# Kernel tuning notes

Measured on AMD Instinct MI355X. Metric: run time of the kernel, lower is better.

## Reference

```python
import jax, jax.numpy as jnp
import numpy as np

B, C, COUT, HEADS = 1, 256, 256, 8
H, W, KS = 96, 96, 7  # spatial dims and neighborhood kernel size


def _nbr_1d(n, k):
    # NATTEN/flex-mask style clamped window: center = clip(q, wl, n-1-wr)
    wl = k // 2
    wr = k // 2 + (k % 2 - 1)
    q = np.arange(n)
    center = np.clip(q, wl, n - 1 - wr)
    start = center - wl  # in [0, n-k]; window always fully in-bounds
    return start[:, None] + np.arange(k)[None, :]  # [n, k]


def _nbr_idx(h, w, k):
    ih = _nbr_1d(h, k)  # [h, k]
    iw = _nbr_1d(w, k)  # [w, k]
    flat = ih[:, None, :, None] * w + iw[None, :, None, :]  # [h, w, k, k]
    return jnp.asarray(flat.reshape(h * w, k * k))  # [S, K]


def setup_inputs() -> dict:
    key = jax.random.key(0)
    ks = jax.random.split(key, 4)
    x = jax.random.normal(ks[0], (B, C, H, W), jnp.float32)
    w_qkv = jax.random.normal(ks[1], (3 * C, C), jnp.float32) * (C ** -0.5)
    b_qkv = jnp.zeros((3 * C,), jnp.float32)
    w_out = jax.random.normal(ks[2], (COUT, C), jnp.float32) * (C ** -0.5)
    b_out = jnp.zeros((COUT,), jnp.float32)
    return {"x": x, "w_qkv": w_qkv, "b_qkv": b_qkv, "w_out": w_out, "b_out": b_out}


def reference(x, w_qkv, b_qkv, w_out, b_out):
    dh = C // HEADS
    S = H * W
    xl = jnp.moveaxis(x, 1, -1)  # [B,H,W,C]
    qkv = xl @ w_qkv.T + b_qkv  # [B,H,W,3C], layout (qkv, heads, dh) on last axis
    qkv = qkv.reshape(B, S, 3, HEADS, dh)
    q = jnp.transpose(qkv[:, :, 0], (0, 2, 1, 3))  # [B,heads,S,dh]
    k = jnp.transpose(qkv[:, :, 1], (0, 2, 1, 3))
    v = jnp.transpose(qkv[:, :, 2], (0, 2, 1, 3))
    # rope_embed_fraction = 0.0 -> RoPE is identity
    nbr = _nbr_idx(H, W, KS)  # [S, K] static neighbor indices, K = KS*KS
    k_nb = jnp.take(k, nbr, axis=2)  # [B,heads,S,K,dh]
    v_nb = jnp.take(v, nbr, axis=2)  # [B,heads,S,K,dh]
    scores = jnp.einsum('bhsd,bhskd->bhsk', q, k_nb) * (dh ** -0.5)
    attn = jax.nn.softmax(scores, axis=-1)  # window fully in-bounds -> no mask
    out = jnp.einsum('bhsk,bhskd->bhsd', attn, v_nb)  # [B,heads,S,dh]
    out = jnp.transpose(out, (0, 2, 1, 3)).reshape(B, S, HEADS * dh)
    out = out @ w_out.T + b_out  # [B,S,COUT]
    out = out.reshape(B, H, W, COUT)
    return jnp.moveaxis(out, -1, 1)  # [B,COUT,H,W]
```

## Files before the change

### kernel.cpp

```cpp
#include <hip/hip_runtime.h>
#include <hip/hip_bf16.h>
#include <math.h>

#define SD 9216
#define HH 96
#define CC 256
#define NO 768
#define NH 8
#define DH 32
#define NW1 (NO * CC)
#define NWT (NW1 + CC * CC)
#define PROW 232

typedef short bf16x8 __attribute__((ext_vector_type(8)));
typedef short short8v __attribute__((ext_vector_type(8)));
typedef float f32x4 __attribute__((ext_vector_type(4)));
typedef unsigned short us8 __attribute__((ext_vector_type(8)));

__device__ __forceinline__ float bf2f(unsigned short u) {
  union { unsigned u; float f; } c; c.u = ((unsigned)u) << 16; return c.f;
}
__device__ __forceinline__ unsigned short f2bf(float f) {
  unsigned u = __float_as_uint(f);
  unsigned r = (u + 0x7FFF + ((u >> 16) & 1)) >> 16;
  return (unsigned short)r;
}

__global__ __launch_bounds__(256) void prep(const float* __restrict__ x,
                                            const float* __restrict__ wq,
                                            const float* __restrict__ wo,
                                            unsigned short* __restrict__ xbt,
                                            unsigned short* __restrict__ wdst) {
  __shared__ float tile[32][33];
  const int b = blockIdx.x;
  const int t = threadIdx.x;
  if (b < 2304) {
    const int s0 = (b % 288) * 32;
    const int c0 = (b / 288) * 32;
    {
      const int c = t >> 3, s4 = (t & 7) * 4;
      const float4 v = *(const float4*)(x + (size_t)(c0 + c) * SD + s0 + s4);
      tile[c][s4] = v.x; tile[c][s4 + 1] = v.y; tile[c][s4 + 2] = v.z; tile[c][s4 + 3] = v.w;
    }
    __syncthreads();
    {
      const int s = t >> 3, c4 = (t & 7) * 4;
      ushort4 o;
      o.x = f2bf(tile[c4][s]);     o.y = f2bf(tile[c4 + 1][s]);
      o.z = f2bf(tile[c4 + 2][s]); o.w = f2bf(tile[c4 + 3][s]);
      *(ushort4*)(xbt + (size_t)(s0 + s) * CC + c0 + c4) = o;
    }
  } else {
    const int i = ((b - 2304) * 256 + t) * 4;
    if (i < NWT) {
      const float* src = (i < NW1) ? (wq + i) : (wo + (i - NW1));
      const float4 v = *(const float4*)src;
      ushort4 o;
      o.x = f2bf(v.x); o.y = f2bf(v.y); o.z = f2bf(v.z); o.w = f2bf(v.w);
      *(ushort4*)(wdst + i) = o;
    }
  }
}

template <int EPI>
__global__ __launch_bounds__(256) void gemm_mfma(const unsigned short* __restrict__ A,
                                                 const unsigned short* __restrict__ Bm,
                                                 const float* __restrict__ bias,
                                                 void* __restrict__ out) {
  __shared__ short Asd[128 * 40];
  __shared__ short Bsd[128 * 40];
  const int t = threadIdx.x;
  const int m0 = blockIdx.x * 128;
  const int n0 = blockIdx.y * 128;
  const int lane = t & 63;
  const int w = t >> 6;
  const int wm = (w >> 1) * 64, wn = (w & 1) * 64;
  f32x4 acc[4][4] = {};
  const int r0 = t >> 2, c16 = (t & 3) * 8;

  for (int k0 = 0; k0 < CC; k0 += 32) {
#pragma unroll
    for (int i = 0; i < 2; ++i) {
      const int r = i * 64 + r0;
      *(int4*)&Asd[r * 40 + c16] = *(const int4*)(A + (size_t)(m0 + r) * CC + k0 + c16);
      *(int4*)&Bsd[r * 40 + c16] = *(const int4*)(Bm + (size_t)(n0 + r) * CC + k0 + c16);
    }
    __syncthreads();
    const int lr = lane & 15, lk = (lane >> 4) * 8;
    bf16x8 af[4], bf[4];
#pragma unroll
    for (int i = 0; i < 4; ++i) af[i] = *(const bf16x8*)&Asd[(wm + i * 16 + lr) * 40 + lk];
#pragma unroll
    for (int j = 0; j < 4; ++j) bf[j] = *(const bf16x8*)&Bsd[(wn + j * 16 + lr) * 40 + lk];
#pragma unroll
    for (int i = 0; i < 4; ++i)
#pragma unroll
      for (int j = 0; j < 4; ++j)
        acc[i][j] = __builtin_amdgcn_mfma_f32_16x16x32_bf16(af[i], bf[j], acc[i][j], 0, 0, 0);
    __syncthreads();
  }

  const int lc = lane & 15, lr4 = (lane >> 4) * 4;
  if (EPI == 0) {
    unsigned short* O = (unsigned short*)out;
#pragma unroll
    for (int i = 0; i < 4; ++i)
#pragma unroll
      for (int j = 0; j < 4; ++j) {
        const int oo = n0 + wn + j * 16 + lc;
        const float bb = bias[oo];
#pragma unroll
        for (int r = 0; r < 4; ++r) {
          const int ss = m0 + wm + i * 16 + lr4 + r;
          O[(size_t)ss * NO + oo] = f2bf(acc[i][j][r] + bb);
        }
      }
  } else {
    float* O = (float*)out;
#pragma unroll
    for (int i = 0; i < 4; ++i)
#pragma unroll
      for (int j = 0; j < 4; ++j) {
#pragma unroll
        for (int r = 0; r < 4; ++r) {
          const int oo = m0 + wm + i * 16 + lr4 + r;
          const int ss = n0 + wn + j * 16 + lc;
          O[(size_t)oo * SD + ss] = acc[i][j][r] + bias[oo];
        }
      }
  }
}

__global__ __launch_bounds__(256) void nattn_mfma(const unsigned short* __restrict__ qkv,
                                                  unsigned short* __restrict__ att) {
  __shared__ short Vt[32][PROW];
  __shared__ short Ps[4][16][PROW];
  const int t = threadIdx.x;
  const int lane = t & 63;
  const int w = t >> 6;
  const int g = lane >> 4;
  const int qcol = lane & 15;
  const int tile = blockIdx.x;
  const int h = blockIdx.y;
  const int ti = tile / 12, tj = tile % 12;
  const int qi0 = ti * 8, qj0 = tj * 8;
  const int ri0 = min(max(qi0, 3), 92) - 3;
  const int cj0 = min(max(qj0, 3), 92) - 3;

  if (t < 224) {
    const int kg4 = t >> 2, dg = t & 3, d0 = dg * 8;
    unsigned short vv[4][8];
#pragma unroll
    for (int kk = 0; kk < 4; ++kk) {
      const int ku = kg4 * 4 + kk;
      if (ku < 196) {
        const unsigned ru = (unsigned)ku / 14u, cu = (unsigned)ku % 14u;
        const int ur = min(ri0 + (int)ru, 95), uc = min(cj0 + (int)cu, 95);
        const us8 vrow = *(const us8*)(qkv + (size_t)(ur * HH + uc) * NO + 2 * CC + h * DH + d0);
#pragma unroll
        for (int jj = 0; jj < 8; ++jj) vv[kk][jj] = vrow[jj];
      } else {
#pragma unroll
        for (int jj = 0; jj < 8; ++jj) vv[kk][jj] = 0;
      }
    }
#pragma unroll
    for (int jj = 0; jj < 8; ++jj) {
      ushort4 o; o.x = vv[0][jj]; o.y = vv[1][jj]; o.z = vv[2][jj]; o.w = vv[3][jj];
      *(ushort4*)&Vt[d0 + jj][kg4 * 4] = o;
    }
  }

  const int ql = w * 16 + qcol;
  const int qi = qi0 + (ql >> 3), qj = qj0 + (ql & 7);
  const int dr = min(max(qi, 3), 92) - 3 - ri0;
  const int dc = min(max(qj, 3), 92) - 3 - cj0;

  const bf16x8 qf = *(const bf16x8*)(qkv + (size_t)(qi * HH + qj) * NO + h * DH + g * 8);

  f32x4 c[13];
#pragma unroll
  for (int m = 0; m < 13; ++m) {
    const int ku = min(16 * m + qcol, 195);
    const unsigned ru = (unsigned)ku / 14u, cu = (unsigned)ku % 14u;
    const int ur = min(ri0 + (int)ru, 95), uc = min(cj0 + (int)cu, 95);
    const bf16x8 kf = *(const bf16x8*)(qkv + (size_t)(ur * HH + uc) * NO + CC + h * DH + g * 8);
    c[m] = __builtin_amdgcn_mfma_f32_16x16x32_bf16(kf, qf, (f32x4){0.f, 0.f, 0.f, 0.f}, 0, 0, 0);
  }

  float mx = -1e30f;
#pragma unroll
  for (int m = 0; m < 13; ++m)
#pragma unroll
    for (int r = 0; r < 4; ++r) {
      const int ku = 16 * m + 4 * g + r;
      const unsigned ru = (unsigned)ku / 14u, cu = (unsigned)ku % 14u;
      const bool ok = (ku < 196) && ((unsigned)((int)ru - dr) <= 6u) && ((unsigned)((int)cu - dc) <= 6u);
      const float s = ok ? c[m][r] * 0.17677669529663687f : -1e30f;
      c[m][r] = s;
      mx = fmaxf(mx, s);
    }
  mx = fmaxf(mx, __shfl_xor(mx, 16));
  mx = fmaxf(mx, __shfl_xor(mx, 32));
  float sum = 0.f;
#pragma unroll
  for (int m = 0; m < 13; ++m)
#pragma unroll
    for (int r = 0; r < 4; ++r) { const float p = __expf(c[m][r] - mx); c[m][r] = p; sum += p; }
  sum += __shfl_xor(sum, 16);
  sum += __shfl_xor(sum, 32);
  const float inv = 1.0f / sum;

#pragma unroll
  for (int m = 0; m < 13; ++m) {
    ushort4 pk;
    pk.x = f2bf(c[m][0] * inv); pk.y = f2bf(c[m][1] * inv);
    pk.z = f2bf(c[m][2] * inv); pk.w = f2bf(c[m][3] * inv);
    *(ushort4*)&Ps[w][qcol][16 * m + 4 * g] = pk;
  }
  if (lane < 32) {
    const short8v z = {0, 0, 0, 0, 0, 0, 0, 0};
    *(short8v*)&Ps[w][lane >> 1][208 + (lane & 1) * 8] = z;
  }
  __syncthreads();

  f32x4 o0 = {0.f, 0.f, 0.f, 0.f}, o1 = {0.f, 0.f, 0.f, 0.f};
#pragma unroll
  for (int tt = 0; tt < 7; ++tt) {
    const bf16x8 pa = *(const bf16x8*)&Ps[w][qcol][tt * 32 + g * 8];
    const bf16x8 v0 = *(const bf16x8*)&Vt[qcol][tt * 32 + g * 8];
    const bf16x8 v1 = *(const bf16x8*)&Vt[16 + qcol][tt * 32 + g * 8];
    o0 = __builtin_amdgcn_mfma_f32_16x16x32_bf16(pa, v0, o0, 0, 0, 0);
    o1 = __builtin_amdgcn_mfma_f32_16x16x32_bf16(pa, v1, o1, 0, 0, 0);
  }

#pragma unroll
  for (int r = 0; r < 4; ++r) {
    const int qlr = w * 16 + g * 4 + r;
    const int s = (qi0 + (qlr >> 3)) * HH + qj0 + (qlr & 7);
    unsigned short* ap = att + (size_t)s * CC + h * DH;
    ap[qcol] = f2bf(o0[r]);
    ap[16 + qcol] = f2bf(o1[r]);
  }
}

extern "C" void kernel_launch(void* const* d_in, const int* in_sizes, int n_in,
                              void* d_out, int out_size, void* d_ws, size_t ws_size,
                              hipStream_t stream) {
  const float* x     = (const float*)d_in[0];
  const float* w_qkv = (const float*)d_in[1];
  const float* b_qkv = (const float*)d_in[2];
  const float* w_out = (const float*)d_in[3];
  const float* b_out = (const float*)d_in[4];
  float* out = (float*)d_out;

  unsigned short* ws   = (unsigned short*)d_ws;
  unsigned short* xbt  = ws;
  unsigned short* wqb  = xbt + (size_t)SD * CC;
  unsigned short* wob  = wqb + (size_t)NO * CC;
  unsigned short* qkvb = wob + (size_t)CC * CC;
  unsigned short* attb = qkvb + (size_t)SD * NO;

  prep<<<dim3(2304 + NWT / 4 / 256), dim3(256), 0, stream>>>(x, w_qkv, w_out, xbt, wqb);

  gemm_mfma<0><<<dim3(SD / 128, NO / 128), dim3(256), 0, stream>>>(xbt, wqb, b_qkv, qkvb);

  nattn_mfma<<<dim3(144, NH), dim3(256), 0, stream>>>(qkvb, attb);

  gemm_mfma<1><<<dim3(CC / 128, SD / 128), dim3(256), 0, stream>>>(wob, attb, b_out, out);
}
```

Baseline: 118.0 us.

## Load GEMM tiles directly to LDS with XOR-swizzled layout and wider K step

```diff
diff --git a/kernel.cpp b/kernel.cpp
--- a/kernel.cpp
+++ b/kernel.cpp
@@ -24,6 +24,11 @@
   unsigned u = __float_as_uint(f);
   unsigned r = (u + 0x7FFF + ((u >> 16) & 1)) >> 16;
   return (unsigned short)r;
+}
+__device__ __forceinline__ void gll16(const unsigned short* g, short* l) {
+  __builtin_amdgcn_global_load_lds(
+      (const __attribute__((address_space(1))) void*)g,
+      (__attribute__((address_space(3))) void*)l, 16, 0, 0);
 }
 
 __global__ __launch_bounds__(256) void prep(const float* __restrict__ x,
@@ -62,41 +67,59 @@
   }
 }
 
-template <int EPI>
-__global__ __launch_bounds__(256) void gemm_mfma(const unsigned short* __restrict__ A,
-                                                 const unsigned short* __restrict__ Bm,
-                                                 const float* __restrict__ bias,
-                                                 void* __restrict__ out) {
-  __shared__ short Asd[128 * 40];
-  __shared__ short Bsd[128 * 40];
+template <int BM, int BN, int EPI>
+__global__ __launch_bounds__(256) void gemm_gll(const unsigned short* __restrict__ A,
+                                                const unsigned short* __restrict__ Bm,
+                                                const float* __restrict__ bias,
+                                                void* __restrict__ out) {
+  constexpr int MI = BM / 32, NJ = BN / 32;
+  __shared__ short Asd[BM * 64];
+  __shared__ short Bsd[BN * 64];
   const int t = threadIdx.x;
-  const int m0 = blockIdx.x * 128;
-  const int n0 = blockIdx.y * 128;
   const int lane = t & 63;
   const int w = t >> 6;
-  const int wm = (w >> 1) * 64, wn = (w & 1) * 64;
-  f32x4 acc[4][4] = {};
-  const int r0 = t >> 2, c16 = (t & 3) * 8;
-
-  for (int k0 = 0; k0 < CC; k0 += 32) {
-#pragma unroll
-    for (int i = 0; i < 2; ++i) {
-      const int r = i * 64 + r0;
-      *(int4*)&Asd[r * 40 + c16] = *(const int4*)(A + (size_t)(m0 + r) * CC + k0 + c16);
-      *(int4*)&Bsd[r * 40 + c16] = *(const int4*)(Bm + (size_t)(n0 + r) * CC + k0 + c16);
+  const int m0 = blockIdx.x * BM;
+  const int n0 = blockIdx.y * BN;
+  const int wm = (w >> 1) * (BM / 2);
+  const int wn = (w & 1) * (BN / 2);
+  f32x4 acc[MI][NJ] = {};
+  const int l8 = lane >> 3;
+  const int sl = lane & 7;
+
+  for (int k0 = 0; k0 < CC; k0 += 64) {
+#pragma unroll
+    for (int q = 0; q < BM / 32; ++q) {
+      const int r = w * (BM / 4) + q * 8 + l8;
+      const int cs = sl ^ (r & 7);
+      gll16(A + (size_t)(m0 + r) * CC + k0 + cs * 8, Asd + (w * (BM / 4) + q * 8) * 64);
+    }
+#pragma unroll
+    for (int q = 0; q < BN / 32; ++q) {
+      const int r = w * (BN / 4) + q * 8 + l8;
+      const int cs = sl ^ (r & 7);
+      gll16(Bm + (size_t)(n0 + r) * CC + k0 + cs * 8, Bsd + (w * (BN / 4) + q * 8) * 64);
     }
     __syncthreads();
-    const int lr = lane & 15, lk = (lane >> 4) * 8;
-    bf16x8 af[4], bf[4];
-#pragma unroll
-    for (int i = 0; i < 4; ++i) af[i] = *(const bf16x8*)&Asd[(wm + i * 16 + lr) * 40 + lk];
-#pragma unroll
-    for (int j = 0; j < 4; ++j) bf[j] = *(const bf16x8*)&Bsd[(wn + j * 16 + lr) * 40 + lk];
-#pragma unroll
-    for (int i = 0; i < 4; ++i)
-#pragma unroll
-      for (int j = 0; j < 4; ++j)
-        acc[i][j] = __builtin_amdgcn_mfma_f32_16x16x32_bf16(af[i], bf[j], acc[i][j], 0, 0, 0);
+    const int lr = lane & 15, g = lane >> 4;
+#pragma unroll
+    for (int kk = 0; kk < 2; ++kk) {
+      bf16x8 af[MI], bf[NJ];
+#pragma unroll
+      for (int i = 0; i < MI; ++i) {
+        const int row = wm + i * 16 + lr;
+        af[i] = *(const bf16x8*)&Asd[row * 64 + ((kk * 4 + g) ^ (lr & 7)) * 8];
+      }
+#pragma unroll
+      for (int j = 0; j < NJ; ++j) {
+        const int row = wn + j * 16 + lr;
+        bf[j] = *(const bf16x8*)&Bsd[row * 64 + ((kk * 4 + g) ^ (lr & 7)) * 8];
+      }
+#pragma unroll
+      for (int i = 0; i < MI; ++i)
+#pragma unroll
+        for (int j = 0; j < NJ; ++j)
+          acc[i][j] = __builtin_amdgcn_mfma_f32_16x16x32_bf16(af[i], bf[j], acc[i][j], 0, 0, 0);
+    }
     __syncthreads();
   }
 
@@ -104,9 +127,9 @@
   if (EPI == 0) {
     unsigned short* O = (unsigned short*)out;
 #pragma unroll
-    for (int i = 0; i < 4; ++i)
-#pragma unroll
-      for (int j = 0; j < 4; ++j) {
+    for (int i = 0; i < MI; ++i)
+#pragma unroll
+      for (int j = 0; j < NJ; ++j) {
         const int oo = n0 + wn + j * 16 + lc;
         const float bb = bias[oo];
 #pragma unroll
@@ -118,9 +141,9 @@
   } else {
     float* O = (float*)out;
 #pragma unroll
-    for (int i = 0; i < 4; ++i)
-#pragma unroll
-      for (int j = 0; j < 4; ++j) {
+    for (int i = 0; i < MI; ++i)
+#pragma unroll
+      for (int j = 0; j < NJ; ++j) {
 #pragma unroll
         for (int r = 0; r < 4; ++r) {
           const int oo = m0 + wm + i * 16 + lr4 + r;
@@ -263,9 +286,9 @@
 
   prep<<<dim3(2304 + NWT / 4 / 256), dim3(256), 0, stream>>>(x, w_qkv, w_out, xbt, wqb);
 
-  gemm_mfma<0><<<dim3(SD / 128, NO / 128), dim3(256), 0, stream>>>(xbt, wqb, b_qkv, qkvb);
+  gemm_gll<128, 128, 0><<<dim3(SD / 128, NO / 128), dim3(256), 0, stream>>>(xbt, wqb, b_qkv, qkvb);
 
   nattn_mfma<<<dim3(144, NH), dim3(256), 0, stream>>>(qkvb, attb);
 
-  gemm_mfma<1><<<dim3(CC / 128, SD / 128), dim3(256), 0, stream>>>(wob, attb, b_out, out);
-}
+  gemm_gll<64, 128, 1><<<dim3(CC / 64, SD / 128), dim3(256), 0, stream>>>(wob, attb, b_out, out);
+}
```

New measurement: 108.0 us. 8.5% less time.
